# Kernel optimization log

Hardware: AMD Instinct MI355X
Metric: run time of the kernel (lower is better)

The kernel has to match this reference:

```python
import jax, jax.numpy as jnp
import numpy as np
import math

E, K = 8, 4
IN, OUT = 768, 768
B, S = 16, 512

def _nearest_factors(n):
    r = int(math.sqrt(n))
    while n % r != 0:
        r -= 1
    r = max(r, 1)
    return r, n // r

D1, D2 = _nearest_factors(IN)      # 24, 32
DO1, DO2 = _nearest_factors(OUT)   # 24, 32

def _cv_squared(v):
    v = v.astype(jnp.float32)
    return jnp.var(v, ddof=1) / (jnp.mean(v) ** 2 + 1e-10)

def setup_inputs() -> dict:
    key = jax.random.key(0)
    ks = jax.random.split(key, 8)
    eye = lambda d: jnp.broadcast_to(jnp.eye(d, dtype=jnp.float32), (E, d, d))
    return {
        "x": jax.random.normal(ks[0], (B, S, IN), jnp.float32),
        "w_gate": 0.02 * jax.random.normal(ks[1], (IN, E), jnp.float32),
        "weight": 0.02 * jax.random.normal(ks[2], (E, OUT, IN), jnp.float32),
        "res_weight": 0.02 * jax.random.normal(ks[3], (OUT, IN), jnp.float32),
        "curve1_in": eye(D1) + 0.01 * jax.random.normal(ks[4], (E, D1, D1), jnp.float32),
        "curve2_in": eye(D2) + 0.01 * jax.random.normal(ks[5], (E, D2, D2), jnp.float32),
        "curve1_out": eye(DO1) + 0.01 * jax.random.normal(ks[6], (E, DO1, DO1), jnp.float32),
        "curve2_out": eye(DO2) + 0.01 * jax.random.normal(ks[7], (E, DO2, DO2), jnp.float32),
    }

def reference(x, w_gate, weight, res_weight, curve1_in, curve2_in, curve1_out, curve2_out):
    b = x.shape[0]
    # ---- noisy_top_k_gating (eval mode: clean logits, no noise) ----
    xm = x.mean(-2)                         # [B, IN]
    logits = xm @ w_gate                    # [B, E]
    top_vals, top_idx = jax.lax.top_k(logits, min(K + 1, E))
    tk_vals = top_vals[:, :K]
    tk_idx = top_idx[:, :K]
    tk_gates = jax.nn.softmax(tk_vals, axis=1)
    gates = jnp.zeros_like(logits).at[jnp.arange(b)[:, None], tk_idx].set(tk_gates)
    load = (gates > 0).sum(0)               # eval: gates_to_load
    importance = gates.sum(0)
    loss = 0.01 * (_cv_squared(importance) + _cv_squared(load))
    # ---- curve-factor expert weight composition (k*2 >= n_experts branch) ----
    rtw = (weight - res_weight).reshape(E, DO1, DO2, D1, D2)
    rtw = jnp.einsum('bij,bjklm->biklm', curve1_out, rtw)
    rtw = jnp.einsum('bik,bjklm->bjilm', curve2_out, rtw)
    rtw = jnp.einsum('bil,bjklm->bjkim', curve1_in, rtw)
    rtw = jnp.einsum('bim,bjklm->bjkli', curve2_in, rtw)
    rtw = rtw.reshape(E, OUT, IN)
    # dropout p=0.1 is identity in eval mode
    expert_weights = res_weight + 0.9 * jnp.sum(rtw[None] * gates[:, :, None, None], axis=1)  # [B, OUT, IN]
    y = jnp.einsum('bsj,bkj->bsk', x, expert_weights)  # [B, S, OUT]
    return y, loss
```

## Files before the change

### kernel.cpp

```cpp
#include <hip/hip_runtime.h>
#include <hip/hip_bf16.h>
#include <hip/hip_cooperative_groups.h>

namespace cg = cooperative_groups;

typedef unsigned short u16;
typedef __attribute__((ext_vector_type(8))) short bf16x8;
typedef __attribute__((ext_vector_type(4))) float f32x4;

#define NE 8
#define NTOPK 4
#define NIN 768
#define NOUT 768
#define NB 16
#define NS 512
#define YSZ (NB * NS * NOUT)
#define EWN (NOUT * NIN)
#define NBLK 768

#define OFF_PART  0u
#define OFF_GATES 3145728u
#define OFF_XBF   3146240u
#define OFF_WD    15729152u
#define OFF_T1T   25166336u
#define OFF_RTW   34603520u
#define OFF_EW    44040704u

#define PRE_BAR(N) asm volatile("s_waitcnt vmcnt(" #N ")\n\ts_barrier" ::: "memory")
#define POST_BAR() asm volatile("s_waitcnt lgkmcnt(0)\n\ts_barrier" ::: "memory")

__device__ __forceinline__ u16 f2bf(float f) {
  union { float f; unsigned u; } v; v.f = f;
  unsigned r = v.u + 0x7fffu + ((v.u >> 16) & 1u);
  return (u16)(r >> 16);
}
__device__ __forceinline__ float bf2f(u16 h) {
  union { unsigned u; float f; } v; v.u = ((unsigned)h) << 16;
  return v.f;
}
__device__ __forceinline__ unsigned cvt2(float a, float b) {
  unsigned r;
  asm("v_cvt_pk_bf16_f32 %0, %1, %2" : "=v"(r) : "v"(a), "v"(b));
  return r;
}
__device__ __forceinline__ void gload16(const void* g, void* l) {
  __builtin_amdgcn_global_load_lds(
      (const __attribute__((address_space(1))) unsigned int*)g,
      (__attribute__((address_space(3))) unsigned int*)l, 16, 0, 0);
}
__device__ __forceinline__ void storeC(float* p, float v) { *p = v; }
__device__ __forceinline__ void storeC(u16* p, float v) { *p = f2bf(v); }

__device__ __forceinline__ void body_xmwd(int u, const float* __restrict__ x,
                                          float* __restrict__ part, u16* __restrict__ xbf,
                                          const float* __restrict__ w,
                                          const float* __restrict__ res,
                                          u16* __restrict__ Wd) {
  if (u < 1024) {
    int t = threadIdx.x;
    if (t < 192) {
      int b = u >> 6;
      int sc = u & 63;
      int c = t * 4;
      float a0 = 0.f, a1 = 0.f, a2 = 0.f, a3 = 0.f;
      int s0 = sc * 8;
#pragma unroll
      for (int r = 0; r < 8; ++r) {
        size_t ro = ((size_t)(b * NS + s0 + r)) * NIN;
        float4 v = *(const float4*)(x + ro + c);
        a0 += v.x; a1 += v.y; a2 += v.z; a3 += v.w;
        ushort4 o;
        o.x = f2bf(v.x); o.y = f2bf(v.y); o.z = f2bf(v.z); o.w = f2bf(v.w);
        *(ushort4*)(xbf + ro + c) = o;
      }
      float4 pv; pv.x = a0; pv.y = a1; pv.z = a2; pv.w = a3;
      *(float4*)(part + (size_t)(b * 64 + sc) * NIN + c) = pv;
    }
  } else {
    int b2 = u - 1024;
    int e = b2 / 288;
    int blk = b2 % 288;
    size_t base = (size_t)blk * 2048 + threadIdx.x * 8;
    float4 wa = *(const float4*)(w + (size_t)e * EWN + base);
    float4 wb = *(const float4*)(w + (size_t)e * EWN + base + 4);
    float4 ra = *(const float4*)(res + base);
    float4 rb = *(const float4*)(res + base + 4);
    bf16x8 o;
    o[0] = (short)f2bf(wa.x - ra.x); o[1] = (short)f2bf(wa.y - ra.y);
    o[2] = (short)f2bf(wa.z - ra.z); o[3] = (short)f2bf(wa.w - ra.w);
    o[4] = (short)f2bf(wb.x - rb.x); o[5] = (short)f2bf(wb.y - rb.y);
    o[6] = (short)f2bf(wb.z - rb.z); o[7] = (short)f2bf(wb.w - rb.w);
    *(bf16x8*)(Wd + (size_t)e * EWN + base) = o;
  }
}

__device__ __forceinline__ void body_logits(int b, float* red,
                                            const float* __restrict__ part,
                                            const float* __restrict__ w_gate,
                                            float* __restrict__ gates_out) {
  int tid = threadIdx.x;
  float p[NE] = {0.f, 0.f, 0.f, 0.f, 0.f, 0.f, 0.f, 0.f};
  for (int i = tid; i < NIN; i += 256) {
    float s = 0.f;
#pragma unroll
    for (int sc = 0; sc < 64; ++sc) s += part[(size_t)(b * 64 + sc) * NIN + i];
    float xmv = s * (1.0f / (float)NS);
#pragma unroll
    for (int e = 0; e < NE; ++e) p[e] += xmv * w_gate[i * NE + e];
  }
#pragma unroll
  for (int e = 0; e < NE; ++e) {
    float v = p[e];
    for (int off = 32; off; off >>= 1) v += __shfl_down(v, off);
    if ((tid & 63) == 0) red[(tid >> 6) * NE + e] = v;
  }
  __syncthreads();
  if (tid == 0) {
    float v[NE]; bool used[NE];
    for (int e = 0; e < NE; ++e) {
      v[e] = red[e] + red[NE + e] + red[2 * NE + e] + red[3 * NE + e];
      used[e] = false;
    }
    int idxs[NTOPK]; float vals[NTOPK];
    for (int t = 0; t < NTOPK; ++t) {
      int best = 0; float bv = -3.4e38f;
      for (int e = 0; e < NE; ++e)
        if (!used[e] && v[e] > bv) { bv = v[e]; best = e; }
      used[best] = true; idxs[t] = best; vals[t] = bv;
    }
    float m = vals[0];
    float ex[NTOPK]; float se = 0.f;
    for (int t = 0; t < NTOPK; ++t) { ex[t] = expf(vals[t] - m); se += ex[t]; }
    float g[NE];
    for (int e = 0; e < NE; ++e) g[e] = 0.f;
    for (int t = 0; t < NTOPK; ++t) g[idxs[t]] = ex[t] / se;
    for (int e = 0; e < NE; ++e) gates_out[b * NE + e] = g[e];
  }
}

__device__ __forceinline__ void body_kron(int bid, u16* lb,
                                          const float* __restrict__ c1,
                                          const float* __restrict__ c2,
                                          const u16* __restrict__ B,
                                          u16* __restrict__ C) {
  const int tid = threadIdx.x;
  const int lane = tid & 63;
  const int w = tid >> 6;
  const int wr = w >> 1, wc = w & 1;
  const int fr = lane & 15;
  const int kq = lane >> 4;
  const int swz = (bid & 7) * 72 + (bid >> 3);
  const int mb = swz % 12;
  const int nb = (swz / 12) % 6;
  const int e = swz / 72;
  const int m0 = mb * 64, n0 = nb * 128;
  const u16* Bb = B + (size_t)e * EWN;
  const float* c1b = c1 + e * 24 * 24;
  const float* c2b = c2 + e * 32 * 32;
  const int r1a = (m0 >> 5) + wr;
  float c2r[2][8];
  {
    const float* p0 = c2b + fr * 32 + kq * 8;
    const float* p1 = c2b + (16 + fr) * 32 + kq * 8;
#pragma unroll
    for (int j = 0; j < 8; ++j) { c2r[0][j] = p0[j]; c2r[1][j] = p1[j]; }
  }
  const int ob1 = (w * 2) * 1024 + lane * 16;
  const int ob2 = ob1 + 1024;
  const int rowB1 = ob1 >> 6, colB1 = ob1 & 63;
  const int rowB2 = ob2 >> 6, colB2 = ob2 & 63;

  auto STAGE = [&](int t) {
    int s = t & 3;
    int k0 = t * 32;
    gload16((const char*)Bb + ((size_t)(n0 + rowB1) * NIN + k0) * 2 + colB1,
            (char*)(lb + s * 4096) + ob1);
    gload16((const char*)Bb + ((size_t)(n0 + rowB2) * NIN + k0) * 2 + colB2,
            (char*)(lb + s * 4096) + ob2);
  };
  f32x4 acc[2][4] = {};
  auto COMPUTE = [&](int t) {
    int s = t & 3;
    const float ca = c1b[r1a * 24 + t];
    bf16x8 aF[2], bF[4];
#pragma unroll
    for (int m = 0; m < 2; ++m) {
      union { unsigned u[4]; bf16x8 v; } pk;
      pk.u[0] = cvt2(ca * c2r[m][0], ca * c2r[m][1]);
      pk.u[1] = cvt2(ca * c2r[m][2], ca * c2r[m][3]);
      pk.u[2] = cvt2(ca * c2r[m][4], ca * c2r[m][5]);
      pk.u[3] = cvt2(ca * c2r[m][6], ca * c2r[m][7]);
      aF[m] = pk.v;
    }
#pragma unroll
    for (int n = 0; n < 4; ++n)
      bF[n] = *(const bf16x8*)(lb + (size_t)s * 4096 + (wc * 64 + n * 16 + fr) * 32 + kq * 8);
#pragma unroll
    for (int m = 0; m < 2; ++m)
#pragma unroll
      for (int n = 0; n < 4; ++n)
        acc[m][n] = __builtin_amdgcn_mfma_f32_16x16x32_bf16(aF[m], bF[n], acc[m][n], 0, 0, 0);
  };

  STAGE(0); STAGE(1); STAGE(2); STAGE(3);
  for (int i = 0; i < 10; ++i) {
    PRE_BAR(4);
    COMPUTE(2 * i); COMPUTE(2 * i + 1);
    POST_BAR();
    STAGE(2 * i + 4); STAGE(2 * i + 5);
  }
  PRE_BAR(4);  COMPUTE(20); COMPUTE(21);  POST_BAR();
  PRE_BAR(0);  COMPUTE(22); COMPUTE(23);

  u16* Cb = C + (size_t)e * EWN;
#pragma unroll
  for (int m = 0; m < 2; ++m) {
    int rb = m0 + wr * 32 + m * 16 + kq * 4;
#pragma unroll
    for (int n = 0; n < 4; ++n) {
      int col = n0 + wc * 64 + n * 16 + fr;
#pragma unroll
      for (int r = 0; r < 4; ++r)
        storeC(Cb + (size_t)(rb + r) * NIN + col, acc[m][n][r]);
    }
  }
}

__device__ __forceinline__ void body_combine(int bid, float* gsh,
                                             const u16* __restrict__ rtwb,
                                             const float* __restrict__ res,
                                             const float* __restrict__ g,
                                             u16* __restrict__ ew,
                                             float* __restrict__ loss_out) {
  int tid = threadIdx.x;
  if (tid < NB * NE) gsh[tid] = 0.9f * g[tid];
  __syncthreads();
  if (bid == 0 && tid == 0) {
    float imp[NE], ld[NE];
    for (int e = 0; e < NE; ++e) {
      float si = 0.f, sl = 0.f;
      for (int b = 0; b < NB; ++b) {
        float gg = g[b * NE + e];
        si += gg; sl += (gg > 0.f) ? 1.f : 0.f;
      }
      imp[e] = si; ld[e] = sl;
    }
    float loss = 0.f;
    for (int which = 0; which < 2; ++which) {
      const float* a = which ? ld : imp;
      float mean = 0.f;
      for (int e = 0; e < NE; ++e) mean += a[e];
      mean *= (1.0f / NE);
      float var = 0.f;
      for (int e = 0; e < NE; ++e) { float d = a[e] - mean; var += d * d; }
      var *= (1.0f / (NE - 1));
      loss += var / (mean * mean + 1e-10f);
    }
    loss_out[0] = 0.01f * loss;
  }
  size_t base = ((size_t)bid * 256 + tid) * 8;
  float rv[NE][8];
#pragma unroll
  for (int e = 0; e < NE; ++e) {
    bf16x8 v = *(const bf16x8*)(rtwb + (size_t)e * EWN + base);
#pragma unroll
    for (int j = 0; j < 8; ++j) rv[e][j] = bf2f((u16)v[j]);
  }
  float r8[8];
  {
    float4 ra = *(const float4*)(res + base);
    float4 rb = *(const float4*)(res + base + 4);
    r8[0] = ra.x; r8[1] = ra.y; r8[2] = ra.z; r8[3] = ra.w;
    r8[4] = rb.x; r8[5] = rb.y; r8[6] = rb.z; r8[7] = rb.w;
  }
  for (int b = 0; b < NB; ++b) {
    float a[8];
#pragma unroll
    for (int j = 0; j < 8; ++j) a[j] = r8[j];
#pragma unroll
    for (int e = 0; e < NE; ++e) {
      float gg = gsh[b * NE + e];
#pragma unroll
      for (int j = 0; j < 8; ++j) a[j] += gg * rv[e][j];
    }
    bf16x8 o;
#pragma unroll
    for (int j = 0; j < 8; ++j) o[j] = (short)f2bf(a[j]);
    *(bf16x8*)(ew + (size_t)b * EWN + base) = o;
  }
}

__device__ __forceinline__ void body_main(int bid, u16* la, u16* lb,
                                          const u16* __restrict__ A,
                                          const u16* __restrict__ Bw,
                                          float* __restrict__ C) {
  const int tid = threadIdx.x;
  const int lane = tid & 63;
  const int w = tid >> 6;
  const int wr = w >> 1, wc = w & 1;
  const int fr = lane & 15;
  const int kq = lane >> 4;
  const int swz = (bid & 7) * 96 + (bid >> 3);
  const int mb = swz % 8;
  const int nb = (swz / 8) % 6;
  const int b = swz / 48;
  const int m0 = mb * 64, n0 = nb * 128;
  const u16* Ab = A + (size_t)b * NS * NIN;
  const u16* Bb = Bw + (size_t)b * EWN;
  const int obA = tid * 16;
  const int rowA = obA >> 6, colA = obA & 63;
  const int obB1 = (w * 2) * 1024 + lane * 16;
  const int obB2 = obB1 + 1024;
  const int rowB1 = obB1 >> 6, colB1 = obB1 & 63;
  const int rowB2 = obB2 >> 6, colB2 = obB2 & 63;

  auto STAGE = [&](int t) {
    int s = t & 3;
    int k0 = t * 32;
    gload16((const char*)Ab + ((size_t)(m0 + rowA) * NIN + k0) * 2 + colA,
            (char*)(la + s * 2048) + obA);
    gload16((const char*)Bb + ((size_t)(n0 + rowB1) * NIN + k0) * 2 + colB1,
            (char*)(lb + s * 4096) + obB1);
    gload16((const char*)Bb + ((size_t)(n0 + rowB2) * NIN + k0) * 2 + colB2,
            (char*)(lb + s * 4096) + obB2);
  };
  f32x4 acc[2][4] = {};
  auto COMPUTE = [&](int t) {
    int s = t & 3;
    bf16x8 aF[2], bF[4];
#pragma unroll
    for (int m = 0; m < 2; ++m)
      aF[m] = *(const bf16x8*)(la + (size_t)s * 2048 + (wr * 32 + m * 16 + fr) * 32 + kq * 8);
#pragma unroll
    for (int n = 0; n < 4; ++n)
      bF[n] = *(const bf16x8*)(lb + (size_t)s * 4096 + (wc * 64 + n * 16 + fr) * 32 + kq * 8);
#pragma unroll
    for (int m = 0; m < 2; ++m)
#pragma unroll
      for (int n = 0; n < 4; ++n)
        acc[m][n] = __builtin_amdgcn_mfma_f32_16x16x32_bf16(aF[m], bF[n], acc[m][n], 0, 0, 0);
  };

  STAGE(0); STAGE(1); STAGE(2); STAGE(3);
  for (int i = 0; i < 10; ++i) {
    PRE_BAR(6);
    COMPUTE(2 * i); COMPUTE(2 * i + 1);
    POST_BAR();
    STAGE(2 * i + 4); STAGE(2 * i + 5);
  }
  PRE_BAR(6);  COMPUTE(20); COMPUTE(21);  POST_BAR();
  PRE_BAR(0);  COMPUTE(22); COMPUTE(23);

  float* Cb = C + (size_t)b * NS * NOUT;
#pragma unroll
  for (int m = 0; m < 2; ++m) {
    int rb = m0 + wr * 32 + m * 16 + kq * 4;
#pragma unroll
    for (int n = 0; n < 4; ++n) {
      int col = n0 + wc * 64 + n * 16 + fr;
#pragma unroll
      for (int r = 0; r < 4; ++r)
        Cb[(size_t)(rb + r) * NOUT + col] = acc[m][n][r];
    }
  }
}

__global__ __launch_bounds__(256, 3) void mega(const float* __restrict__ x,
                                               const float* __restrict__ w_gate,
                                               const float* __restrict__ weight,
                                               const float* __restrict__ res_w,
                                               const float* __restrict__ c1i,
                                               const float* __restrict__ c2i,
                                               const float* __restrict__ c1o,
                                               const float* __restrict__ c2o,
                                               float* part, float* gates,
                                               u16* xbf, u16* Wd, u16* T1t, u16* rtwb,
                                               u16* ew, float* y, float* lossp) {
  __shared__ __attribute__((aligned(128))) u16 lA0[4 * 64 * 32];
  __shared__ __attribute__((aligned(128))) u16 lB0[4 * 128 * 32];
  cg::grid_group grid = cg::this_grid();
  const int bid = blockIdx.x;

  for (int u = bid; u < 3328; u += NBLK)
    body_xmwd(u, x, part, xbf, weight, res_w, Wd);
  grid.sync();

  if (bid < 576)       body_kron(bid, lB0, c1i, c2i, Wd, T1t);
  else if (bid < 592)  body_logits(bid - 576, (float*)lA0, part, w_gate, gates);
  grid.sync();

  if (bid < 576)       body_kron(bid, lB0, c1o, c2o, T1t, rtwb);
  grid.sync();

  if (bid < 288)       body_combine(bid, (float*)lA0, rtwb, res_w, gates, ew, lossp);
  grid.sync();

  body_main(bid, lA0, lB0, xbf, ew, y);
}

__global__ __launch_bounds__(256) void k_p0(const float* x, float* part, u16* xbf,
                                            const float* w, const float* res, u16* Wd) {
  body_xmwd(blockIdx.x, x, part, xbf, w, res, Wd);
}
__global__ __launch_bounds__(256) void k_p1(const float* c1, const float* c2,
                                            const u16* B, u16* C,
                                            const float* part, const float* w_gate,
                                            float* gates) {
  __shared__ __attribute__((aligned(128))) u16 lB[4 * 128 * 32];
  __shared__ float red[4 * NE];
  if (blockIdx.x < 576) body_kron(blockIdx.x, lB, c1, c2, B, C);
  else                  body_logits(blockIdx.x - 576, red, part, w_gate, gates);
}
__global__ __launch_bounds__(256) void k_p2(const float* c1, const float* c2,
                                            const u16* B, u16* C) {
  __shared__ __attribute__((aligned(128))) u16 lB[4 * 128 * 32];
  body_kron(blockIdx.x, lB, c1, c2, B, C);
}
__global__ __launch_bounds__(256) void k_p3(const u16* rtwb, const float* res,
                                            const float* g, u16* ew, float* loss) {
  __shared__ float gsh[NB * NE];
  body_combine(blockIdx.x, gsh, rtwb, res, g, ew, loss);
}
__global__ __launch_bounds__(256) void k_p4(const u16* A, const u16* Bw, float* C) {
  __shared__ __attribute__((aligned(128))) u16 lA[4 * 64 * 32];
  __shared__ __attribute__((aligned(128))) u16 lB[4 * 128 * 32];
  body_main(blockIdx.x, lA, lB, A, Bw, C);
}

extern "C" void kernel_launch(void* const* d_in, const int* in_sizes, int n_in,
                              void* d_out, int out_size, void* d_ws, size_t ws_size,
                              hipStream_t stream) {
  const float* x = (const float*)d_in[0];
  const float* w_gate = (const float*)d_in[1];
  const float* weight = (const float*)d_in[2];
  const float* res_w = (const float*)d_in[3];
  const float* c1i = (const float*)d_in[4];
  const float* c2i = (const float*)d_in[5];
  const float* c1o = (const float*)d_in[6];
  const float* c2o = (const float*)d_in[7];

  char* ws = (char*)d_ws;
  float* part = (float*)(ws + OFF_PART);
  float* gates = (float*)(ws + OFF_GATES);
  u16* xbf = (u16*)(ws + OFF_XBF);
  u16* Wd = (u16*)(ws + OFF_WD);
  u16* T1t = (u16*)(ws + OFF_T1T);
  u16* rtwb = (u16*)(ws + OFF_RTW);
  u16* ew = (u16*)(ws + OFF_EW);

  float* y = (float*)d_out;
  float* loss = y + YSZ;

  int occ = 0;
  bool coop =
      (hipOccupancyMaxActiveBlocksPerMultiprocessor(&occ, mega, 256, 0) == hipSuccess) &&
      occ >= 3;
  if (coop) {
    void* args[] = {(void*)&x, (void*)&w_gate, (void*)&weight, (void*)&res_w,
                    (void*)&c1i, (void*)&c2i, (void*)&c1o, (void*)&c2o,
                    (void*)&part, (void*)&gates, (void*)&xbf, (void*)&Wd,
                    (void*)&T1t, (void*)&rtwb, (void*)&ew, (void*)&y, (void*)&loss};
    coop = (hipLaunchCooperativeKernel((const void*)mega, dim3(NBLK), dim3(256),
                                       args, 0, stream) == hipSuccess);
  }
  if (!coop) {
    k_p0<<<dim3(3328), 256, 0, stream>>>(x, part, xbf, weight, res_w, Wd);
    k_p1<<<dim3(592), 256, 0, stream>>>(c1i, c2i, Wd, T1t, part, w_gate, gates);
    k_p2<<<dim3(576), 256, 0, stream>>>(c1o, c2o, T1t, rtwb);
    k_p3<<<dim3(288), 256, 0, stream>>>(rtwb, res_w, gates, ew, loss);
    k_p4<<<dim3(768), 256, 0, stream>>>(xbf, ew, y);
  }
}
```

Baseline: 77.65 us.

## Split main GEMM out of cooperative kernel and use 128x128 tiles

Moves the final batched GEMM out of the cooperative mega kernel into its own launch, dropping the last grid sync. The new kernel uses 128x128 output tiles over 384 blocks instead of 64x128 over 768, raising data reuse per block and freeing the mega kernel from the GEMM's shared-memory and register needs. The cost is an extra kernel launch, larger LDS and accumulator footprint per block, and fewer blocks to fill the GPU.

```diff
diff --git a/kernel.cpp b/kernel.cpp
--- a/kernel.cpp
+++ b/kernel.cpp
@@ -185,11 +185,12 @@
     bf16x8 aF[2], bF[4];
 #pragma unroll
     for (int m = 0; m < 2; ++m) {
+      const float* cr = c2r[m];
       union { unsigned u[4]; bf16x8 v; } pk;
-      pk.u[0] = cvt2(ca * c2r[m][0], ca * c2r[m][1]);
-      pk.u[1] = cvt2(ca * c2r[m][2], ca * c2r[m][3]);
-      pk.u[2] = cvt2(ca * c2r[m][4], ca * c2r[m][5]);
-      pk.u[3] = cvt2(ca * c2r[m][6], ca * c2r[m][7]);
+      pk.u[0] = cvt2(ca * cr[0], ca * cr[1]);
+      pk.u[1] = cvt2(ca * cr[2], ca * cr[3]);
+      pk.u[2] = cvt2(ca * cr[4], ca * cr[5]);
+      pk.u[3] = cvt2(ca * cr[6], ca * cr[7]);
       aF[m] = pk.v;
     }
 #pragma unroll
@@ -290,81 +291,6 @@
   }
 }
 
-__device__ __forceinline__ void body_main(int bid, u16* la, u16* lb,
-                                          const u16* __restrict__ A,
-                                          const u16* __restrict__ Bw,
-                                          float* __restrict__ C) {
-  const int tid = threadIdx.x;
-  const int lane = tid & 63;
-  const int w = tid >> 6;
-  const int wr = w >> 1, wc = w & 1;
-  const int fr = lane & 15;
-  const int kq = lane >> 4;
-  const int swz = (bid & 7) * 96 + (bid >> 3);
-  const int mb = swz % 8;
-  const int nb = (swz / 8) % 6;
-  const int b = swz / 48;
-  const int m0 = mb * 64, n0 = nb * 128;
-  const u16* Ab = A + (size_t)b * NS * NIN;
-  const u16* Bb = Bw + (size_t)b * EWN;
-  const int obA = tid * 16;
-  const int rowA = obA >> 6, colA = obA & 63;
-  const int obB1 = (w * 2) * 1024 + lane * 16;
-  const int obB2 = obB1 + 1024;
-  const int rowB1 = obB1 >> 6, colB1 = obB1 & 63;
-  const int rowB2 = obB2 >> 6, colB2 = obB2 & 63;
-
-  auto STAGE = [&](int t) {
-    int s = t & 3;
-    int k0 = t * 32;
-    gload16((const char*)Ab + ((size_t)(m0 + rowA) * NIN + k0) * 2 + colA,
-            (char*)(la + s * 2048) + obA);
-    gload16((const char*)Bb + ((size_t)(n0 + rowB1) * NIN + k0) * 2 + colB1,
-            (char*)(lb + s * 4096) + obB1);
-    gload16((const char*)Bb + ((size_t)(n0 + rowB2) * NIN + k0) * 2 + colB2,
-            (char*)(lb + s * 4096) + obB2);
-  };
-  f32x4 acc[2][4] = {};
-  auto COMPUTE = [&](int t) {
-    int s = t & 3;
-    bf16x8 aF[2], bF[4];
-#pragma unroll
-    for (int m = 0; m < 2; ++m)
-      aF[m] = *(const bf16x8*)(la + (size_t)s * 2048 + (wr * 32 + m * 16 + fr) * 32 + kq * 8);
-#pragma unroll
-    for (int n = 0; n < 4; ++n)
-      bF[n] = *(const bf16x8*)(lb + (size_t)s * 4096 + (wc * 64 + n * 16 + fr) * 32 + kq * 8);
-#pragma unroll
-    for (int m = 0; m < 2; ++m)
-#pragma unroll
-      for (int n = 0; n < 4; ++n)
-        acc[m][n] = __builtin_amdgcn_mfma_f32_16x16x32_bf16(aF[m], bF[n], acc[m][n], 0, 0, 0);
-  };
-
-  STAGE(0); STAGE(1); STAGE(2); STAGE(3);
-  for (int i = 0; i < 10; ++i) {
-    PRE_BAR(6);
-    COMPUTE(2 * i); COMPUTE(2 * i + 1);
-    POST_BAR();
-    STAGE(2 * i + 4); STAGE(2 * i + 5);
-  }
-  PRE_BAR(6);  COMPUTE(20); COMPUTE(21);  POST_BAR();
-  PRE_BAR(0);  COMPUTE(22); COMPUTE(23);
-
-  float* Cb = C + (size_t)b * NS * NOUT;
-#pragma unroll
-  for (int m = 0; m < 2; ++m) {
-    int rb = m0 + wr * 32 + m * 16 + kq * 4;
-#pragma unroll
-    for (int n = 0; n < 4; ++n) {
-      int col = n0 + wc * 64 + n * 16 + fr;
-#pragma unroll
-      for (int r = 0; r < 4; ++r)
-        Cb[(size_t)(rb + r) * NOUT + col] = acc[m][n][r];
-    }
-  }
-}
-
 __global__ __launch_bounds__(256, 3) void mega(const float* __restrict__ x,
                                                const float* __restrict__ w_gate,
                                                const float* __restrict__ weight,
@@ -375,9 +301,9 @@
                                                const float* __restrict__ c2o,
                                                float* part, float* gates,
                                                u16* xbf, u16* Wd, u16* T1t, u16* rtwb,
-                                               u16* ew, float* y, float* lossp) {
-  __shared__ __attribute__((aligned(128))) u16 lA0[4 * 64 * 32];
+                                               u16* ew, float* lossp) {
   __shared__ __attribute__((aligned(128))) u16 lB0[4 * 128 * 32];
+  __shared__ float red[NB * NE];
   cg::grid_group grid = cg::this_grid();
   const int bid = blockIdx.x;
 
@@ -386,16 +312,89 @@
   grid.sync();
 
   if (bid < 576)       body_kron(bid, lB0, c1i, c2i, Wd, T1t);
-  else if (bid < 592)  body_logits(bid - 576, (float*)lA0, part, w_gate, gates);
+  else if (bid < 592)  body_logits(bid - 576, red, part, w_gate, gates);
   grid.sync();
 
   if (bid < 576)       body_kron(bid, lB0, c1o, c2o, T1t, rtwb);
   grid.sync();
 
-  if (bid < 288)       body_combine(bid, (float*)lA0, rtwb, res_w, gates, ew, lossp);
-  grid.sync();
-
-  body_main(bid, lA0, lB0, xbf, ew, y);
+  if (bid < 288)       body_combine(bid, red, rtwb, res_w, gates, ew, lossp);
+}
+
+__global__ __launch_bounds__(256, 2) void k_main(const u16* __restrict__ A,
+                                                 const u16* __restrict__ Bw,
+                                                 float* __restrict__ C) {
+  __shared__ __attribute__((aligned(128))) u16 la[4 * 128 * 32];
+  __shared__ __attribute__((aligned(128))) u16 lb[4 * 128 * 32];
+  const int tid = threadIdx.x;
+  const int lane = tid & 63;
+  const int w = tid >> 6;
+  const int wr = w >> 1, wc = w & 1;
+  const int fr = lane & 15;
+  const int kq = lane >> 4;
+  const int swz = (blockIdx.x & 7) * 48 + (blockIdx.x >> 3);
+  const int mb = swz % 4;
+  const int nb = (swz / 4) % 6;
+  const int b = swz / 24;
+  const int m0 = mb * 128, n0 = nb * 128;
+  const u16* Ab = A + (size_t)b * NS * NIN;
+  const u16* Bb = Bw + (size_t)b * EWN;
+  const int ob1 = tid * 16;
+  const int ob2 = ob1 + 4096;
+  const int row1 = ob1 >> 6, col1 = ob1 & 63;
+  const int row2 = ob2 >> 6, col2 = ob2 & 63;
+
+  auto STAGE = [&](int t) {
+    int s = t & 3;
+    int k0 = t * 32;
+    gload16((const char*)Ab + ((size_t)(m0 + row1) * NIN + k0) * 2 + col1,
+            (char*)(la + s * 4096) + ob1);
+    gload16((const char*)Ab + ((size_t)(m0 + row2) * NIN + k0) * 2 + col2,
+            (char*)(la + s * 4096) + ob2);
+    gload16((const char*)Bb + ((size_t)(n0 + row1) * NIN + k0) * 2 + col1,
+            (char*)(lb + s * 4096) + ob1);
+    gload16((const char*)Bb + ((size_t)(n0 + row2) * NIN + k0) * 2 + col2,
+            (char*)(lb + s * 4096) + ob2);
+  };
+  f32x4 acc[4][4] = {};
+  auto COMPUTE = [&](int t) {
+    int s = t & 3;
+    bf16x8 aF[4], bF[4];
+#pragma unroll
+    for (int m = 0; m < 4; ++m)
+      aF[m] = *(const bf16x8*)(la + (size_t)s * 4096 + (wr * 64 + m * 16 + fr) * 32 + kq * 8);
+#pragma unroll
+    for (int n = 0; n < 4; ++n)
+      bF[n] = *(const bf16x8*)(lb + (size_t)s * 4096 + (wc * 64 + n * 16 + fr) * 32 + kq * 8);
+#pragma unroll
+    for (int m = 0; m < 4; ++m)
+#pragma unroll
+      for (int n = 0; n < 4; ++n)
+        acc[m][n] = __builtin_amdgcn_mfma_f32_16x16x32_bf16(aF[m], bF[n], acc[m][n], 0, 0, 0);
+  };
+
+  STAGE(0); STAGE(1); STAGE(2); STAGE(3);
+  for (int i = 0; i < 10; ++i) {
+    PRE_BAR(8);
+    COMPUTE(2 * i); COMPUTE(2 * i + 1);
+    POST_BAR();
+    STAGE(2 * i + 4); STAGE(2 * i + 5);
+  }
+  PRE_BAR(8);  COMPUTE(20); COMPUTE(21);  POST_BAR();
+  PRE_BAR(0);  COMPUTE(22); COMPUTE(23);
+
+  float* Cb = C + (size_t)b * NS * NOUT;
+#pragma unroll
+  for (int m = 0; m < 4; ++m) {
+    int rb = m0 + wr * 64 + m * 16 + kq * 4;
+#pragma unroll
+    for (int n = 0; n < 4; ++n) {
+      int col = n0 + wc * 64 + n * 16 + fr;
+#pragma unroll
+      for (int r = 0; r < 4; ++r)
+        Cb[(size_t)(rb + r) * NOUT + col] = acc[m][n][r];
+    }
+  }
 }
 
 __global__ __launch_bounds__(256) void k_p0(const float* x, float* part, u16* xbf,
@@ -407,7 +406,7 @@
                                             const float* part, const float* w_gate,
                                             float* gates) {
   __shared__ __attribute__((aligned(128))) u16 lB[4 * 128 * 32];
-  __shared__ float red[4 * NE];
+  __shared__ float red[NB * NE];
   if (blockIdx.x < 576) body_kron(blockIdx.x, lB, c1, c2, B, C);
   else                  body_logits(blockIdx.x - 576, red, part, w_gate, gates);
 }
@@ -420,11 +419,6 @@
                                             const float* g, u16* ew, float* loss) {
   __shared__ float gsh[NB * NE];
   body_combine(blockIdx.x, gsh, rtwb, res, g, ew, loss);
-}
-__global__ __launch_bounds__(256) void k_p4(const u16* A, const u16* Bw, float* C) {
-  __shared__ __attribute__((aligned(128))) u16 lA[4 * 64 * 32];
-  __shared__ __attribute__((aligned(128))) u16 lB[4 * 128 * 32];
-  body_main(blockIdx.x, lA, lB, A, Bw, C);
 }
 
 extern "C" void kernel_launch(void* const* d_in, const int* in_sizes, int n_in,
@@ -459,7 +453,7 @@
     void* args[] = {(void*)&x, (void*)&w_gate, (void*)&weight, (void*)&res_w,
                     (void*)&c1i, (void*)&c2i, (void*)&c1o, (void*)&c2o,
                     (void*)&part, (void*)&gates, (void*)&xbf, (void*)&Wd,
-                    (void*)&T1t, (void*)&rtwb, (void*)&ew, (void*)&y, (void*)&loss};
+                    (void*)&T1t, (void*)&rtwb, (void*)&ew, (void*)&loss};
     coop = (hipLaunchCooperativeKernel((const void*)mega, dim3(NBLK), dim3(256),
                                        args, 0, stream) == hipSuccess);
   }
@@ -468,6 +462,6 @@
     k_p1<<<dim3(592), 256, 0, stream>>>(c1i, c2i, Wd, T1t, part, w_gate, gates);
     k_p2<<<dim3(576), 256, 0, stream>>>(c1o, c2o, T1t, rtwb);
     k_p3<<<dim3(288), 256, 0, stream>>>(rtwb, res_w, gates, ew, loss);
-    k_p4<<<dim3(768), 256, 0, stream>>>(xbf, ew, y);
-  }
-}
+  }
+  k_main<<<dim3(384), 256, 0, stream>>>(xbf, ew, y);
+}
```

New measurement: 77.09 us. About the same (-0.7%).
